# Performance work log

Measured on AMD Instinct MI355X. Metric: run time of the kernel, lower is better.

The kernel has to match this reference:

```python
import jax, jax.numpy as jnp
import numpy as np

B, IN, HID, EMB, K = 65536, 256, 256, 64, 4096
EPS = 1e-5  # BatchNorm1d default eps


def setup_inputs() -> dict:
    key = jax.random.key(0)
    ks = jax.random.split(key, 12)
    s = 0.05
    return {
        "x": jax.random.normal(ks[0], (B, IN), jnp.float32),
        "W1": jax.random.normal(ks[1], (HID, IN), jnp.float32) * s,
        "b1": jax.random.normal(ks[2], (HID,), jnp.float32) * s,
        "gamma": jnp.ones((HID,), jnp.float32),
        "beta": jnp.zeros((HID,), jnp.float32),
        "mean": jax.random.normal(ks[3], (HID,), jnp.float32) * s,
        "var": jax.random.uniform(ks[4], (HID,), jnp.float32, 0.5, 1.5),
        "W2": jax.random.normal(ks[5], (HID // 2, HID), jnp.float32) * s,
        "b2": jax.random.normal(ks[6], (HID // 2,), jnp.float32) * s,
        "W3": jax.random.normal(ks[7], (EMB, HID // 2), jnp.float32) * s,
        "b3": jax.random.normal(ks[8], (EMB,), jnp.float32) * s,
        "codebook": jax.random.normal(ks[9], (K, EMB), jnp.float32),
    }


def reference(x, W1, b1, gamma, beta, mean, var, W2, b2, W3, b3, codebook):
    # encoder: Linear -> BatchNorm1d (eval stats) -> ReLU -> Linear -> ReLU -> Linear -> Tanh
    h = x @ W1.T + b1                                   # [B, HID]
    h = (h - mean) * jax.lax.rsqrt(var + EPS) * gamma + beta
    h = jax.nn.relu(h)
    h = jax.nn.relu(h @ W2.T + b2)                      # [B, HID//2]
    z = jnp.tanh(h @ W3.T + b3)                         # [B, EMB]
    # squared-distance matrix: ||z||^2 + ||e||^2 - 2 z e^T  -> [B, K]
    d = (jnp.sum(z * z, axis=1, keepdims=True)
         + jnp.sum(codebook * codebook, axis=1)
         - 2.0 * (z @ codebook.T))
    return jnp.argmin(d, axis=1)                        # [B] int token indices
```

## Files before the change

kernel.cpp:

```cpp
#include <hip/hip_runtime.h>

#define IN_DIM  256
#define HID_DIM 256
#define H2_DIM  128
#define EMB_DIM 64
#define K_CODES 4096
#define EPS_BN  1e-5f


typedef _Float16 f16;
typedef _Float16 f16x4 __attribute__((ext_vector_type(4)));
typedef _Float16 f16x8 __attribute__((ext_vector_type(8)));
typedef float    f32x16 __attribute__((ext_vector_type(16)));

__global__ __launch_bounds__(256) void k_norms(const float* __restrict__ cb,
                                               float* __restrict__ norms) {
    int c = blockIdx.x * 256 + threadIdx.x;
    const float4* row = reinterpret_cast<const float4*>(cb + (size_t)c * EMB_DIM);
    float s = 0.f;
#pragma unroll
    for (int i = 0; i < EMB_DIM / 4; ++i) {
        float4 v = row[i];
        s += v.x * v.x + v.y * v.y + v.z * v.z + v.w * v.w;
    }
    norms[c] = 0.5f * s;
}

__global__ __launch_bounds__(256) void k_prep(
    const float* __restrict__ W1, const float* __restrict__ W2,
    const float* __restrict__ W3, const float* __restrict__ cb,
    f16* __restrict__ p1h, f16* __restrict__ p1l,
    f16* __restrict__ p2h, f16* __restrict__ p2l,
    f16* __restrict__ p3h, f16* __restrict__ p3l,
    f16* __restrict__ cfh, f16* __restrict__ cfl) {
    int t = blockIdx.x * 256 + threadIdx.x;
    const float* src; f16 *dh, *dl; int tt, row, k0, K;
    if (t < 8192) {
        tt = t; int f = tt >> 6, l = tt & 63;
        int ct = f & 7, kst = f >> 3;
        row = ct * 32 + (l & 31); k0 = kst * 16 + (l >> 5) * 8;
        src = W1; K = IN_DIM; dh = p1h; dl = p1l;
    } else if (t < 12288) {
        tt = t - 8192; int f = tt >> 6, l = tt & 63;
        int ct = f & 3, kst = f >> 2;
        row = ct * 32 + (l & 31); k0 = kst * 16 + (l >> 5) * 8;
        src = W2; K = HID_DIM; dh = p2h; dl = p2l;
    } else if (t < 13312) {
        tt = t - 12288; int f = tt >> 6, l = tt & 63;
        int ct = f & 1, ks = f >> 1;
        row = ct * 32 + (l & 31); k0 = ks * 16 + (l >> 5) * 8;
        src = W3; K = H2_DIM; dh = p3h; dl = p3l;
    } else {
        tt = t - 13312; int f = tt >> 6, l = tt & 63;
        int ct = f & 3, ks = (f >> 2) & 3, ch = f >> 4;
        row = ch * 128 + ct * 32 + (l & 31); k0 = ks * 16 + (l >> 5) * 8;
        src = cb; K = EMB_DIM; dh = cfh; dl = cfl;
    }
    const float* s = src + (size_t)row * K + k0;
    f16x8 hv, lv;
#pragma unroll
    for (int j = 0; j < 8; ++j) {
        float v = s[j];
        f16 h = (f16)v;
        hv[j] = h;
        lv[j] = (f16)(v - (float)h);
    }
    *(f16x8*)(dh + (size_t)tt * 8) = hv;
    *(f16x8*)(dl + (size_t)tt * 8) = lv;
}

__global__ __launch_bounds__(256) void k_encoder_mfma(
    const float* __restrict__ x,
    const f16* __restrict__ p1h, const f16* __restrict__ p1l,
    const f16* __restrict__ p2h, const f16* __restrict__ p2l,
    const f16* __restrict__ p3h, const f16* __restrict__ p3l,
    const float* __restrict__ b1,
    const float* __restrict__ gm, const float* __restrict__ bt,
    const float* __restrict__ mu, const float* __restrict__ vr,
    const float* __restrict__ b2, const float* __restrict__ b3,
    f16* __restrict__ Zh, f16* __restrict__ Zl) {
    __shared__ __align__(16) f16 sm[25600];
    const int tid  = threadIdx.x;
    const int lane = tid & 63;
    const int w    = tid >> 6;
    const int ln31 = lane & 31;
    const int q    = lane >> 5;
    const int r0   = blockIdx.x * 32;

#pragma unroll
    for (int it = 0; it < 8; ++it) {
        int i = it * 256 + tid;
        int row = i >> 6, c4 = (i & 63) * 4;
        float4 v = *reinterpret_cast<const float4*>(
            x + (size_t)(r0 + row) * IN_DIM + c4);
        f16x4 hv, lv;
        hv[0] = (f16)v.x; lv[0] = (f16)(v.x - (float)hv[0]);
        hv[1] = (f16)v.y; lv[1] = (f16)(v.y - (float)hv[1]);
        hv[2] = (f16)v.z; lv[2] = (f16)(v.z - (float)hv[2]);
        hv[3] = (f16)v.w; lv[3] = (f16)(v.w - (float)hv[3]);
        *(f16x4*)(sm + row * 264 + c4)        = hv;
        *(f16x4*)(sm + 8448 + row * 264 + c4) = lv;
    }
    __syncthreads();

    f32x16 acc1a = {};
    f32x16 acc1b = {};
#pragma unroll 2
    for (int kst = 0; kst < 16; ++kst) {
        int koff = kst * 16 + q * 8;
        f16x8 ah = *(const f16x8*)(sm + ln31 * 264 + koff);
        f16x8 al = *(const f16x8*)(sm + 8448 + ln31 * 264 + koff);
        const f16* pbh = p1h + (size_t)(kst * 8 + 2 * w) * 512 + lane * 8;
        const f16* pbl = p1l + (size_t)(kst * 8 + 2 * w) * 512 + lane * 8;
        f16x8 bh0 = *(const f16x8*)pbh;
        f16x8 bh1 = *(const f16x8*)(pbh + 512);
        f16x8 bl0 = *(const f16x8*)pbl;
        f16x8 bl1 = *(const f16x8*)(pbl + 512);
        acc1a = __builtin_amdgcn_mfma_f32_32x32x16_f16(ah, bh0, acc1a, 0, 0, 0);
        acc1b = __builtin_amdgcn_mfma_f32_32x32x16_f16(ah, bh1, acc1b, 0, 0, 0);
        acc1a = __builtin_amdgcn_mfma_f32_32x32x16_f16(al, bh0, acc1a, 0, 0, 0);
        acc1b = __builtin_amdgcn_mfma_f32_32x32x16_f16(al, bh1, acc1b, 0, 0, 0);
        acc1a = __builtin_amdgcn_mfma_f32_32x32x16_f16(ah, bl0, acc1a, 0, 0, 0);
        acc1b = __builtin_amdgcn_mfma_f32_32x32x16_f16(ah, bl1, acc1b, 0, 0, 0);
    }
    __syncthreads();

    {
#pragma unroll
        for (int nt = 0; nt < 2; ++nt) {
            int j = w * 64 + nt * 32 + ln31;
            float sc = gm[j] * rsqrtf(vr[j] + EPS_BN);
            float sh = (b1[j] - mu[j]) * sc + bt[j];
            const f32x16& a = nt ? acc1b : acc1a;
#pragma unroll
            for (int r = 0; r < 16; ++r) {
                int row = (r & 3) + 8 * (r >> 2) + 4 * q;
                float v = a[r] * sc + sh;
                v = v > 0.f ? v : 0.f;
                f16 h = (f16)v;
                sm[row * 264 + j]        = h;
                sm[8448 + row * 264 + j] = (f16)(v - (float)h);
            }
        }
    }
    __syncthreads();

    f32x16 acc2a = {};
    f32x16 acc2b = {};
#pragma unroll 2
    for (int kst = 0; kst < 16; ++kst) {
        int koff = kst * 16 + q * 8;
        f16x8 ah = *(const f16x8*)(sm + ln31 * 264 + koff);
        f16x8 al = *(const f16x8*)(sm + 8448 + ln31 * 264 + koff);
        const f16* pbh = p2h + (size_t)(kst * 4 + w) * 512 + lane * 8;
        const f16* pbl = p2l + (size_t)(kst * 4 + w) * 512 + lane * 8;
        f16x8 bh = *(const f16x8*)pbh;
        f16x8 bl = *(const f16x8*)pbl;
        f32x16& acc = (kst & 1) ? acc2b : acc2a;
        acc = __builtin_amdgcn_mfma_f32_32x32x16_f16(ah, bh, acc, 0, 0, 0);
        acc = __builtin_amdgcn_mfma_f32_32x32x16_f16(al, bh, acc, 0, 0, 0);
        acc = __builtin_amdgcn_mfma_f32_32x32x16_f16(ah, bl, acc, 0, 0, 0);
    }
    {
        int j2 = w * 32 + ln31;
        float bias = b2[j2];
#pragma unroll
        for (int r = 0; r < 16; ++r) {
            int row = (r & 3) + 8 * (r >> 2) + 4 * q;
            float v = (acc2a[r] + acc2b[r]) + bias;
            v = v > 0.f ? v : 0.f;
            f16 h = (f16)v;
            sm[16896 + row * 136 + j2] = h;
            sm[21248 + row * 136 + j2] = (f16)(v - (float)h);
        }
    }
    __syncthreads();

    if (w < 2) {
        f32x16 acc3a = {};
        f32x16 acc3b = {};
#pragma unroll 2
        for (int ks = 0; ks < 8; ++ks) {
            f16x8 ah = *(const f16x8*)(sm + 16896 + ln31 * 136 + ks * 16 + q * 8);
            f16x8 al = *(const f16x8*)(sm + 21248 + ln31 * 136 + ks * 16 + q * 8);
            const f16* pbh = p3h + (size_t)(ks * 2 + w) * 512 + lane * 8;
            const f16* pbl = p3l + (size_t)(ks * 2 + w) * 512 + lane * 8;
            f16x8 bh = *(const f16x8*)pbh;
            f16x8 bl = *(const f16x8*)pbl;
            f32x16& acc = (ks & 1) ? acc3b : acc3a;
            acc = __builtin_amdgcn_mfma_f32_32x32x16_f16(ah, bh, acc, 0, 0, 0);
            acc = __builtin_amdgcn_mfma_f32_32x32x16_f16(al, bh, acc, 0, 0, 0);
            acc = __builtin_amdgcn_mfma_f32_32x32x16_f16(ah, bl, acc, 0, 0, 0);
        }
        int j3 = w * 32 + ln31;
        float bias = b3[j3];
#pragma unroll
        for (int r = 0; r < 16; ++r) {
            int row = (r & 3) + 8 * (r >> 2) + 4 * q;
            float zv = tanhf((acc3a[r] + acc3b[r]) + bias);
            f16 h = (f16)zv;
            size_t idx = (size_t)(r0 + row) * EMB_DIM + j3;
            Zh[idx] = h;
            Zl[idx] = (f16)(zv - (float)h);
        }
    }
}

__global__ __launch_bounds__(256) void k_argmin_mfma(
    const f16* __restrict__ Zh, const f16* __restrict__ Zl,
    const f16* __restrict__ cfh, const f16* __restrict__ cfl,
    const float* __restrict__ norms, int* __restrict__ out) {
    __shared__ __align__(16) f16 sm[16896];
    f16* ebh = sm;
    f16* ebl = sm + 8192;
    float* nbuf = (float*)(sm + 16384);
    const int tid  = threadIdx.x;
    const int lane = tid & 63;
    const int w    = tid >> 6;
    const int ln31 = lane & 31;
    const int q    = lane >> 5;
    const int r0   = blockIdx.x * 128;

    f16x8 ah[4], al[4];
#pragma unroll
    for (int ks = 0; ks < 4; ++ks) {
        size_t zoff = (size_t)(r0 + w * 32 + ln31) * EMB_DIM + ks * 16 + q * 8;
        ah[ks] = *(const f16x8*)(Zh + zoff);
        al[ks] = *(const f16x8*)(Zl + zoff);
    }

    float bv[16];
    int   bi[16];
#pragma unroll
    for (int i = 0; i < 16; ++i) { bv[i] = -3.4e38f; bi[i] = 0; }

    for (int ch = 0; ch < K_CODES / 128; ++ch) {
        __syncthreads();
        const float4* sh = (const float4*)(cfh + (size_t)ch * 8192);
        const float4* sl = (const float4*)(cfl + (size_t)ch * 8192);
        float4* dh = (float4*)ebh;
        float4* dl = (float4*)ebl;
#pragma unroll
        for (int it = 0; it < 4; ++it) {
            dh[it * 256 + tid] = sh[it * 256 + tid];
            dl[it * 256 + tid] = sl[it * 256 + tid];
        }
        if (tid < 128) nbuf[tid] = norms[ch * 128 + tid];
        __syncthreads();

#pragma unroll 1
        for (int ct = 0; ct < 4; ++ct) {
            f16x8 bh[4], bl[4];
#pragma unroll
            for (int ks = 0; ks < 4; ++ks) {
                int off = (ks * 4 + ct) * 512 + lane * 8;
                bh[ks] = *(const f16x8*)(ebh + off);
                bl[ks] = *(const f16x8*)(ebl + off);
            }
            f32x16 acc0 = {};
            f32x16 acc1 = {};
#pragma unroll
            for (int ks = 0; ks < 4; ks += 2) {
                acc0 = __builtin_amdgcn_mfma_f32_32x32x16_f16(ah[ks],     bh[ks],     acc0, 0, 0, 0);
                acc1 = __builtin_amdgcn_mfma_f32_32x32x16_f16(ah[ks + 1], bh[ks + 1], acc1, 0, 0, 0);
                acc0 = __builtin_amdgcn_mfma_f32_32x32x16_f16(al[ks],     bh[ks],     acc0, 0, 0, 0);
                acc1 = __builtin_amdgcn_mfma_f32_32x32x16_f16(al[ks + 1], bh[ks + 1], acc1, 0, 0, 0);
                acc0 = __builtin_amdgcn_mfma_f32_32x32x16_f16(ah[ks],     bl[ks],     acc0, 0, 0, 0);
                acc1 = __builtin_amdgcn_mfma_f32_32x32x16_f16(ah[ks + 1], bl[ks + 1], acc1, 0, 0, 0);
            }
            float nv  = nbuf[ct * 32 + ln31];
            int   col = ch * 128 + ct * 32 + ln31;
#pragma unroll
            for (int r = 0; r < 16; ++r) {
                float t  = (acc0[r] + acc1[r]) - nv;
                bool  gt = t > bv[r];
                bv[r] = gt ? t : bv[r];
                bi[r] = gt ? col : bi[r];
            }
        }
    }

    __syncthreads();
    float* redv = (float*)sm;
    int*   redi = (int*)sm + 4224;
#pragma unroll
    for (int r = 0; r < 16; ++r) {
        int row = (r & 3) + 8 * (r >> 2) + 4 * q + 32 * w;
        redv[row * 33 + ln31] = bv[r];
        redi[row * 33 + ln31] = bi[r];
    }
    __syncthreads();
    if (tid < 128) {
        float v  = redv[tid * 33];
        int   ix = redi[tid * 33];
#pragma unroll
        for (int j = 1; j < 32; ++j) {
            float vj = redv[tid * 33 + j];
            int   ij = redi[tid * 33 + j];
            if (vj > v) { v = vj; ix = ij; }
        }
        out[r0 + tid] = ix;
    }
}

extern "C" void kernel_launch(void* const* d_in, const int* in_sizes, int n_in,
                              void* d_out, int out_size, void* d_ws, size_t ws_size,
                              hipStream_t stream) {
    (void)n_in; (void)out_size; (void)ws_size;
    const float* x  = (const float*)d_in[0];
    const float* W1 = (const float*)d_in[1];
    const float* b1 = (const float*)d_in[2];
    const float* gm = (const float*)d_in[3];
    const float* bt = (const float*)d_in[4];
    const float* mu = (const float*)d_in[5];
    const float* vr = (const float*)d_in[6];
    const float* W2 = (const float*)d_in[7];
    const float* b2 = (const float*)d_in[8];
    const float* W3 = (const float*)d_in[9];
    const float* b3 = (const float*)d_in[10];
    const float* cb = (const float*)d_in[11];

    char* ws = (char*)d_ws;
    float* norms = (float*)ws;
    f16* cfh = (f16*)(ws + 16384);
    f16* cfl = (f16*)(ws + 540672);
    f16* p1h = (f16*)(ws + 1064960);
    f16* p1l = (f16*)(ws + 1196032);
    f16* p2h = (f16*)(ws + 1327104);
    f16* p2l = (f16*)(ws + 1392640);
    f16* p3h = (f16*)(ws + 1458176);
    f16* p3l = (f16*)(ws + 1474560);
    f16* Zh  = (f16*)(ws + 1490944);
    f16* Zl  = (f16*)(ws + 9879552);
    int* out = (int*)d_out;

    const int B = in_sizes[0] / IN_DIM;

    k_norms<<<K_CODES / 256, 256, 0, stream>>>(cb, norms);
    k_prep<<<180, 256, 0, stream>>>(W1, W2, W3, cb, p1h, p1l, p2h, p2l,
                                    p3h, p3l, cfh, cfl);
    k_encoder_mfma<<<B / 32, 256, 0, stream>>>(x, p1h, p1l, p2h, p2l, p3h, p3l,
                                               b1, gm, bt, mu, vr, b2, b3, Zh, Zl);
    k_argmin_mfma<<<B / 128, 256, 0, stream>>>(Zh, Zl, cfh, cfl, norms, out);
}
```

Baseline: 294.6 us.

## Prefetch encoder weight fragments and split argmin code tiles across 8 waves

Encoder GEMM loops now load next-iteration weight fragments from global memory before issuing the current MFMAs, hiding load latency. The argmin kernel doubles its block to 512 threads, with two wave groups each scanning half of the 32-code tiles per chunk, then merges partial best values through shared memory. Tie-breaking toward the lower index is added to match argmin semantics. This adds an extra reduction pass and register pressure, and may lower occupancy.

```diff
diff --git a/kernel.cpp b/kernel.cpp
--- a/kernel.cpp
+++ b/kernel.cpp
@@ -105,23 +105,31 @@
 
     f32x16 acc1a = {};
     f32x16 acc1b = {};
+    {
+        const f16* q1h = p1h + (size_t)(2 * w) * 512 + lane * 8;
+        const f16* q1l = p1l + (size_t)(2 * w) * 512 + lane * 8;
+        f16x8 bh0 = *(const f16x8*)(q1h);
+        f16x8 bh1 = *(const f16x8*)(q1h + 512);
+        f16x8 bl0 = *(const f16x8*)(q1l);
+        f16x8 bl1 = *(const f16x8*)(q1l + 512);
 #pragma unroll 2
-    for (int kst = 0; kst < 16; ++kst) {
-        int koff = kst * 16 + q * 8;
-        f16x8 ah = *(const f16x8*)(sm + ln31 * 264 + koff);
-        f16x8 al = *(const f16x8*)(sm + 8448 + ln31 * 264 + koff);
-        const f16* pbh = p1h + (size_t)(kst * 8 + 2 * w) * 512 + lane * 8;
-        const f16* pbl = p1l + (size_t)(kst * 8 + 2 * w) * 512 + lane * 8;
-        f16x8 bh0 = *(const f16x8*)pbh;
-        f16x8 bh1 = *(const f16x8*)(pbh + 512);
-        f16x8 bl0 = *(const f16x8*)pbl;
-        f16x8 bl1 = *(const f16x8*)(pbl + 512);
-        acc1a = __builtin_amdgcn_mfma_f32_32x32x16_f16(ah, bh0, acc1a, 0, 0, 0);
-        acc1b = __builtin_amdgcn_mfma_f32_32x32x16_f16(ah, bh1, acc1b, 0, 0, 0);
-        acc1a = __builtin_amdgcn_mfma_f32_32x32x16_f16(al, bh0, acc1a, 0, 0, 0);
-        acc1b = __builtin_amdgcn_mfma_f32_32x32x16_f16(al, bh1, acc1b, 0, 0, 0);
-        acc1a = __builtin_amdgcn_mfma_f32_32x32x16_f16(ah, bl0, acc1a, 0, 0, 0);
-        acc1b = __builtin_amdgcn_mfma_f32_32x32x16_f16(ah, bl1, acc1b, 0, 0, 0);
+        for (int kst = 0; kst < 16; ++kst) {
+            f16x8 ch0 = bh0, ch1 = bh1, cl0 = bl0, cl1 = bl1;
+            int kn = (kst + 1) & 15;
+            bh0 = *(const f16x8*)(q1h + (size_t)kn * 4096);
+            bh1 = *(const f16x8*)(q1h + (size_t)kn * 4096 + 512);
+            bl0 = *(const f16x8*)(q1l + (size_t)kn * 4096);
+            bl1 = *(const f16x8*)(q1l + (size_t)kn * 4096 + 512);
+            int koff = kst * 16 + q * 8;
+            f16x8 ah = *(const f16x8*)(sm + ln31 * 264 + koff);
+            f16x8 al = *(const f16x8*)(sm + 8448 + ln31 * 264 + koff);
+            acc1a = __builtin_amdgcn_mfma_f32_32x32x16_f16(ah, ch0, acc1a, 0, 0, 0);
+            acc1b = __builtin_amdgcn_mfma_f32_32x32x16_f16(ah, ch1, acc1b, 0, 0, 0);
+            acc1a = __builtin_amdgcn_mfma_f32_32x32x16_f16(al, ch0, acc1a, 0, 0, 0);
+            acc1b = __builtin_amdgcn_mfma_f32_32x32x16_f16(al, ch1, acc1b, 0, 0, 0);
+            acc1a = __builtin_amdgcn_mfma_f32_32x32x16_f16(ah, cl0, acc1a, 0, 0, 0);
+            acc1b = __builtin_amdgcn_mfma_f32_32x32x16_f16(ah, cl1, acc1b, 0, 0, 0);
+        }
     }
     __syncthreads();
 
@@ -147,19 +155,25 @@
 
     f32x16 acc2a = {};
     f32x16 acc2b = {};
+    {
+        const f16* q2h = p2h + (size_t)w * 512 + lane * 8;
+        const f16* q2l = p2l + (size_t)w * 512 + lane * 8;
+        f16x8 bh = *(const f16x8*)(q2h);
+        f16x8 bl = *(const f16x8*)(q2l);
 #pragma unroll 2
-    for (int kst = 0; kst < 16; ++kst) {
-        int koff = kst * 16 + q * 8;
-        f16x8 ah = *(const f16x8*)(sm + ln31 * 264 + koff);
-        f16x8 al = *(const f16x8*)(sm + 8448 + ln31 * 264 + koff);
-        const f16* pbh = p2h + (size_t)(kst * 4 + w) * 512 + lane * 8;
-        const f16* pbl = p2l + (size_t)(kst * 4 + w) * 512 + lane * 8;
-        f16x8 bh = *(const f16x8*)pbh;
-        f16x8 bl = *(const f16x8*)pbl;
-        f32x16& acc = (kst & 1) ? acc2b : acc2a;
-        acc = __builtin_amdgcn_mfma_f32_32x32x16_f16(ah, bh, acc, 0, 0, 0);
-        acc = __builtin_amdgcn_mfma_f32_32x32x16_f16(al, bh, acc, 0, 0, 0);
-        acc = __builtin_amdgcn_mfma_f32_32x32x16_f16(ah, bl, acc, 0, 0, 0);
+        for (int kst = 0; kst < 16; ++kst) {
+            f16x8 cbh = bh, cbl = bl;
+            int kn = (kst + 1) & 15;
+            bh = *(const f16x8*)(q2h + (size_t)kn * 2048);
+            bl = *(const f16x8*)(q2l + (size_t)kn * 2048);
+            int koff = kst * 16 + q * 8;
+            f16x8 ah = *(const f16x8*)(sm + ln31 * 264 + koff);
+            f16x8 al = *(const f16x8*)(sm + 8448 + ln31 * 264 + koff);
+            f32x16& acc = (kst & 1) ? acc2b : acc2a;
+            acc = __builtin_amdgcn_mfma_f32_32x32x16_f16(ah, cbh, acc, 0, 0, 0);
+            acc = __builtin_amdgcn_mfma_f32_32x32x16_f16(al, cbh, acc, 0, 0, 0);
+            acc = __builtin_amdgcn_mfma_f32_32x32x16_f16(ah, cbl, acc, 0, 0, 0);
+        }
     }
     {
         int j2 = w * 32 + ln31;
@@ -179,18 +193,22 @@
     if (w < 2) {
         f32x16 acc3a = {};
         f32x16 acc3b = {};
+        const f16* q3h = p3h + (size_t)w * 512 + lane * 8;
+        const f16* q3l = p3l + (size_t)w * 512 + lane * 8;
+        f16x8 bh = *(const f16x8*)(q3h);
+        f16x8 bl = *(const f16x8*)(q3l);
 #pragma unroll 2
         for (int ks = 0; ks < 8; ++ks) {
+            f16x8 cbh = bh, cbl = bl;
+            int kn = (ks + 1) & 7;
+            bh = *(const f16x8*)(q3h + (size_t)kn * 1024);
+            bl = *(const f16x8*)(q3l + (size_t)kn * 1024);
             f16x8 ah = *(const f16x8*)(sm + 16896 + ln31 * 136 + ks * 16 + q * 8);
             f16x8 al = *(const f16x8*)(sm + 21248 + ln31 * 136 + ks * 16 + q * 8);
-            const f16* pbh = p3h + (size_t)(ks * 2 + w) * 512 + lane * 8;
-            const f16* pbl = p3l + (size_t)(ks * 2 + w) * 512 + lane * 8;
-            f16x8 bh = *(const f16x8*)pbh;
-            f16x8 bl = *(const f16x8*)pbl;
             f32x16& acc = (ks & 1) ? acc3b : acc3a;
-            acc = __builtin_amdgcn_mfma_f32_32x32x16_f16(ah, bh, acc, 0, 0, 0);
-            acc = __builtin_amdgcn_mfma_f32_32x32x16_f16(al, bh, acc, 0, 0, 0);
-            acc = __builtin_amdgcn_mfma_f32_32x32x16_f16(ah, bl, acc, 0, 0, 0);
+            acc = __builtin_amdgcn_mfma_f32_32x32x16_f16(ah, cbh, acc, 0, 0, 0);
+            acc = __builtin_amdgcn_mfma_f32_32x32x16_f16(al, cbh, acc, 0, 0, 0);
+            acc = __builtin_amdgcn_mfma_f32_32x32x16_f16(ah, cbl, acc, 0, 0, 0);
         }
         int j3 = w * 32 + ln31;
         float bias = b3[j3];
@@ -206,7 +224,7 @@
     }
 }
 
-__global__ __launch_bounds__(256) void k_argmin_mfma(
+__global__ __launch_bounds__(512) void k_argmin_mfma(
     const f16* __restrict__ Zh, const f16* __restrict__ Zl,
     const f16* __restrict__ cfh, const f16* __restrict__ cfl,
     const float* __restrict__ norms, int* __restrict__ out) {
@@ -217,6 +235,8 @@
     const int tid  = threadIdx.x;
     const int lane = tid & 63;
     const int w    = tid >> 6;
+    const int rt   = w & 3;
+    const int hp   = w >> 2;
     const int ln31 = lane & 31;
     const int q    = lane >> 5;
     const int r0   = blockIdx.x * 128;
@@ -224,7 +244,7 @@
     f16x8 ah[4], al[4];
 #pragma unroll
     for (int ks = 0; ks < 4; ++ks) {
-        size_t zoff = (size_t)(r0 + w * 32 + ln31) * EMB_DIM + ks * 16 + q * 8;
+        size_t zoff = (size_t)(r0 + rt * 32 + ln31) * EMB_DIM + ks * 16 + q * 8;
         ah[ks] = *(const f16x8*)(Zh + zoff);
         al[ks] = *(const f16x8*)(Zl + zoff);
     }
@@ -241,15 +261,16 @@
         float4* dh = (float4*)ebh;
         float4* dl = (float4*)ebl;
 #pragma unroll
-        for (int it = 0; it < 4; ++it) {
-            dh[it * 256 + tid] = sh[it * 256 + tid];
-            dl[it * 256 + tid] = sl[it * 256 + tid];
+        for (int it = 0; it < 2; ++it) {
+            dh[it * 512 + tid] = sh[it * 512 + tid];
+            dl[it * 512 + tid] = sl[it * 512 + tid];
         }
         if (tid < 128) nbuf[tid] = norms[ch * 128 + tid];
         __syncthreads();
 
 #pragma unroll 1
-        for (int ct = 0; ct < 4; ++ct) {
+        for (int c2 = 0; c2 < 2; ++c2) {
+            int ct = hp * 2 + c2;
             f16x8 bh[4], bl[4];
 #pragma unroll
             for (int ks = 0; ks < 4; ++ks) {
@@ -281,13 +302,39 @@
     }
 
     __syncthreads();
+    {
+        float* pv = (float*)sm;
+        int*   pi = (int*)sm + 4096;
+        if (w >= 4) {
+#pragma unroll
+            for (int r = 0; r < 16; ++r) {
+                pv[(w - 4) * 1024 + lane * 16 + r] = bv[r];
+                pi[(w - 4) * 1024 + lane * 16 + r] = bi[r];
+            }
+        }
+        __syncthreads();
+        if (w < 4) {
+#pragma unroll
+            for (int r = 0; r < 16; ++r) {
+                float v2 = pv[w * 1024 + lane * 16 + r];
+                int   i2 = pi[w * 1024 + lane * 16 + r];
+                bool tk = (v2 > bv[r]) || (v2 == bv[r] && i2 < bi[r]);
+                bv[r] = tk ? v2 : bv[r];
+                bi[r] = tk ? i2 : bi[r];
+            }
+        }
+    }
+    __syncthreads();
+
     float* redv = (float*)sm;
     int*   redi = (int*)sm + 4224;
-#pragma unroll
-    for (int r = 0; r < 16; ++r) {
-        int row = (r & 3) + 8 * (r >> 2) + 4 * q + 32 * w;
-        redv[row * 33 + ln31] = bv[r];
-        redi[row * 33 + ln31] = bi[r];
+    if (w < 4) {
+#pragma unroll
+        for (int r = 0; r < 16; ++r) {
+            int row = (r & 3) + 8 * (r >> 2) + 4 * q + 32 * w;
+            redv[row * 33 + ln31] = bv[r];
+            redi[row * 33 + ln31] = bi[r];
+        }
     }
     __syncthreads();
     if (tid < 128) {
@@ -297,7 +344,7 @@
         for (int j = 1; j < 32; ++j) {
             float vj = redv[tid * 33 + j];
             int   ij = redi[tid * 33 + j];
-            if (vj > v) { v = vj; ix = ij; }
+            if (vj > v || (vj == v && ij < ix)) { v = vj; ix = ij; }
         }
         out[r0 + tid] = ix;
     }
@@ -341,5 +388,5 @@
                                     p3h, p3l, cfh, cfl);
     k_encoder_mfma<<<B / 32, 256, 0, stream>>>(x, p1h, p1l, p2h, p2l, p3h, p3l,
                                                b1, gm, bt, mu, vr, b2, b3, Zh, Zl);
-    k_argmin_mfma<<<B / 128, 256, 0, stream>>>(Zh, Zl, cfh, cfl, norms, out);
-}
+    k_argmin_mfma<<<B / 128, 512, 0, stream>>>(Zh, Zl, cfh, cfl, norms, out);
+}
```

Result: faster. 281.1 us (-4.6%).
